# Performance work log

Measured on AMD Instinct MI355X. Metric: run time of the kernel, lower is better.

Reference implementation:

```python
import jax, jax.numpy as jnp
import numpy as np

DIM = 64
HEADS = 8
DIM_HEAD = 64
INNER = HEADS * DIM_HEAD  # 512
MLP = 256
DEPTH = 4
B = 64
HW = 15
NPATCH = HW * HW  # 225
N = NPATCH + 1    # 226 tokens incl cls
SCALE = DIM_HEAD ** -0.5
EPS = 1e-5


def setup_inputs() -> dict:
    key = jax.random.key(0)
    ks = jax.random.split(key, 20)
    s = 0.02
    inp = {
        "hsi": jax.random.normal(ks[0], (B, DIM, HW, HW), jnp.float32),
        "lidar": jax.random.normal(ks[1], (B, DIM, HW, HW), jnp.float32),
        "cls_hsi": jax.random.normal(ks[2], (1, 1, DIM), jnp.float32),
        "cls_lidar": jax.random.normal(ks[3], (1, 1, DIM), jnp.float32),
        "pos_hsi": jax.random.normal(ks[4], (1, N, DIM), jnp.float32),
        "pos_lidar": jax.random.normal(ks[5], (1, N, DIM), jnp.float32),
        "fmg_w": jax.random.normal(ks[6], (2 * DIM, DIM * DIM), jnp.float32) * s,
        "ln1_g": jnp.ones((DEPTH, DIM), jnp.float32),
        "ln1_b": jnp.zeros((DEPTH, DIM), jnp.float32),
        "qkv_w": jax.random.normal(ks[7], (DEPTH, DIM, 3 * INNER), jnp.float32) * s,
        "out_w": jax.random.normal(ks[8], (DEPTH, INNER, DIM), jnp.float32) * s,
        "out_b": jnp.zeros((DEPTH, DIM), jnp.float32),
        "ln2_g": jnp.ones((DEPTH, DIM), jnp.float32),
        "ln2_b": jnp.zeros((DEPTH, DIM), jnp.float32),
        "ff_w1": jax.random.normal(ks[9], (DEPTH, DIM, MLP), jnp.float32) * s,
        "ff_b1": jnp.zeros((DEPTH, MLP), jnp.float32),
        "ff_w2": jax.random.normal(ks[10], (DEPTH, MLP, DIM), jnp.float32) * s,
        "ff_b2": jnp.zeros((DEPTH, DIM), jnp.float32),
    }
    return inp


def _ln(x, g, b):
    m = x.mean(-1, keepdims=True)
    v = ((x - m) ** 2).mean(-1, keepdims=True)
    return (x - m) * jax.lax.rsqrt(v + EPS) * g + b


def _attn(x, dfm, g, b, wqkv, wo, bo):
    # x: [B, N, DIM]; dfm: [B, DIM_HEAD] diagonal of per-sample fusion matrix
    xn = _ln(x, g, b)
    qkv = xn @ wqkv  # [B, N, 3*INNER]
    q, k, v = jnp.split(qkv, 3, axis=-1)
    def heads(t):
        return t.reshape(B, N, HEADS, DIM_HEAD).transpose(0, 2, 1, 3)  # bhnd
    q, v = heads(q), heads(v)
    # torch.einsum('bhnd,bdd->bhnd', q, fm): repeated 'd' in bdd = diagonal of fm
    k = q * dfm[:, None, None, :]
    dots = jnp.einsum('bhid,bhjd->bhij', q, k) * SCALE
    attn = jax.nn.softmax(dots, axis=-1)
    out = jnp.einsum('bhij,bhjd->bhid', attn, v)
    out = out.transpose(0, 2, 1, 3).reshape(B, N, INNER)
    return out @ wo + bo


def _ff(x, g, b, w1, b1, w2, b2):
    xn = _ln(x, g, b)
    h = jax.nn.gelu(xn @ w1 + b1, approximate=False)
    return h @ w2 + b2


def reference(hsi, lidar, cls_hsi, cls_lidar, pos_hsi, pos_lidar, fmg_w,
              ln1_g, ln1_b, qkv_w, out_w, out_b, ln2_g, ln2_b,
              ff_w1, ff_b1, ff_w2, ff_b2):
    # patch_to_embedding with p1=p2=1: b c h w -> b (h w) c
    h_e = hsi.reshape(B, DIM, NPATCH).transpose(0, 2, 1)
    l_e = lidar.reshape(B, DIM, NPATCH).transpose(0, 2, 1)

    # fusion matrix from pre-exchange embeddings
    x = jnp.concatenate([h_e.mean(1), l_e.mean(1)], axis=-1)  # [B, 2*DIM]
    fm = jax.nn.sigmoid(x @ fmg_w).reshape(B, DIM, DIM)
    dfm = jnp.diagonal(fm, axis1=1, axis2=2)  # [B, DIM]

    # _exchange_embedding (faithful to source: reads both halves from hsi)
    n2 = NPATCH // 2
    h_ex = jnp.concatenate([h_e[:, :n2], h_e[:, n2:]], axis=1)
    l_ex = jnp.concatenate([h_e[:, :n2], h_e[:, n2:]], axis=1)

    h_ex = jnp.concatenate([jnp.broadcast_to(cls_hsi, (B, 1, DIM)), h_ex], axis=1)
    l_ex = jnp.concatenate([jnp.broadcast_to(cls_lidar, (B, 1, DIM)), l_ex], axis=1)
    h_ex = h_ex + pos_hsi[:, :N]
    l_ex = l_ex + pos_lidar[:, :N]

    def run_layers(h, l):
        for i in range(DEPTH):
            h = _attn(h, dfm, ln1_g[i], ln1_b[i], qkv_w[i], out_w[i], out_b[i]) + h
            h = _ff(h, ln2_g[i], ln2_b[i], ff_w1[i], ff_b1[i], ff_w2[i], ff_b2[i]) + h
            l = _attn(l, dfm, ln1_g[i], ln1_b[i], qkv_w[i], out_w[i], out_b[i]) + l
            l = _ff(l, ln2_g[i], ln2_b[i], ff_w1[i], ff_b1[i], ff_w2[i], ff_b2[i]) + l
        return h, l

    h_ex, l_ex = run_layers(h_ex, l_ex)

    # _exchange_token: swap cls tokens
    h_new = jnp.concatenate([l_ex[:, :1], h_ex[:, 1:]], axis=1)
    l_new = jnp.concatenate([h_ex[:, :1], l_ex[:, 1:]], axis=1)

    h_new, l_new = run_layers(h_new, l_new)
    return h_new[:, 0] + l_new[:, 0]
```

## Files before the change

### kernel.cpp

```cpp
#include <hip/hip_runtime.h>
#include <hip/hip_bf16.h>
#include <cstdint>

#define NB 64
#define ND 64
#define NH 8
#define DH 64
#define NIN 512
#define NMLP 256
#define NDEPTH 4
#define NPATCH 225
#define NTOK 226
#define NSB 128
#define NROWS (NSB*NTOK)

#define VP 240
#define PBP 40


typedef __attribute__((ext_vector_type(8))) short bfrag8;
typedef __attribute__((ext_vector_type(4))) float ffrag4;

__device__ __forceinline__ unsigned short f2b(float f) {
  uint32_t u; __builtin_memcpy(&u, &f, 4);
  u += 0x7fff + ((u >> 16) & 1);
  return (unsigned short)(u >> 16);
}

__global__ void k_dfm(const float* __restrict__ hsi, const float* __restrict__ lidar,
                      const float* __restrict__ fsub, float* __restrict__ sdfm) {
  __shared__ float xc[128];
  int b = blockIdx.x, t = threadIdx.x;
  const float* src = (t < 64) ? hsi : lidar;
  int d = t & 63;
  const float* p = src + ((size_t)b * 64 + d) * NPATCH;
  float s = 0.f;
  for (int i = 0; i < NPATCH; ++i) s += p[i];
  xc[t] = s * (1.0f / 225.0f);
  __syncthreads();
  if (t < 64) {
    float acc = 0.f;
    for (int c = 0; c < 128; ++c) acc += xc[c] * fsub[c * 64 + t];
    float sg = 1.0f / (1.0f + expf(-acc));
    sdfm[b * 64 + t] = sqrtf(sg);
  }
}

__global__ __launch_bounds__(256) void k_build(const float* __restrict__ hsi,
                        const float* __restrict__ cls_h, const float* __restrict__ cls_l,
                        const float* __restrict__ pos_h, const float* __restrict__ pos_l,
                        const float* __restrict__ g, const float* __restrict__ bb,
                        float* __restrict__ X, uint16_t* __restrict__ Xn) {
  __shared__ float Xt[113][65];
  int sb = blockIdx.x >> 1, h = blockIdx.x & 1;
  int s = sb >> 6, b = sb & 63;
  int t = threadIdx.x, w = t >> 6, l = t & 63;
  int p0 = h ? 112 : 0;
  int pc = h ? 113 : 112;

  for (int dd = 0; dd < 16; ++dd) {
    int d = w * 16 + dd;
    const float* row = hsi + ((size_t)b * 64 + d) * NPATCH + p0;
    #pragma unroll
    for (int ch = 0; ch < 2; ++ch) {
      int i = ch * 64 + l;
      if (i < pc) Xt[i][d] = row[i];
    }
  }
  __syncthreads();

  int d = l;
  for (int n_loc = w; n_loc <= 112; n_loc += 4) {
    int n = h * 113 + n_loc;
    float v;
    if (n == 0) v = s ? cls_l[d] : cls_h[d];
    else        v = Xt[h ? n_loc : (n_loc - 1)][d];
    v += (s ? pos_l : pos_h)[n * ND + d];
    size_t r = (size_t)sb * NTOK + n;
    X[r * ND + d] = v;
    float sm = v, sq = v * v;
    #pragma unroll
    for (int o = 32; o; o >>= 1) { sm += __shfl_xor(sm, o); sq += __shfl_xor(sq, o); }
    float m = sm * (1.f / 64.f);
    float rs = rsqrtf(sq * (1.f / 64.f) - m * m + 1e-5f);
    Xn[r * ND + d] = f2b((v - m) * rs * g[d] + bb[d]);
  }
}

__global__ __launch_bounds__(256) void k_wconv(
    const float* __restrict__ qkv_w, const float* __restrict__ out_w,
    const float* __restrict__ ff_w1, const float* __restrict__ ff_w2,
    const float* __restrict__ fmg_w,
    uint16_t* __restrict__ Wqv, uint16_t* __restrict__ Wo,
    uint16_t* __restrict__ W1, uint16_t* __restrict__ W2,
    float* __restrict__ fmg_sub) {
  int i = blockIdx.x * 256 + threadIdx.x;
  if (i < 262144) {
    int ly = i >> 16, rem = i & 65535, n = rem >> 6, k = rem & 63;
    int col = n + ((n >> 9) << 9);
    Wqv[i] = f2b(qkv_w[((size_t)ly * 64 + k) * 1536 + col]);
  } else if (i < 393216) {
    int j = i - 262144;
    int ly = j >> 15, rem = j & 32767, n = rem >> 9, k = rem & 511;
    Wo[j] = f2b(out_w[((size_t)ly * 512 + k) * 64 + n]);
  } else if (i < 458752) {
    int j = i - 393216;
    int ly = j >> 14, rem = j & 16383, n = rem >> 6, k = rem & 63;
    W1[j] = f2b(ff_w1[((size_t)ly * 64 + k) * 256 + n]);
  } else if (i < 524288) {
    int j = i - 458752;
    int ly = j >> 14, rem = j & 16383, n = rem >> 8, k = rem & 255;
    W2[j] = f2b(ff_w2[((size_t)ly * 256 + k) * 64 + n]);
  } else {
    int j = i - 524288;
    int c = j >> 6, t = j & 63;
    fmg_sub[j] = fmg_w[(size_t)c * 4096 + t * 65];
  }
}

__global__ __launch_bounds__(512) void k_fattn(const uint16_t* __restrict__ Xn,
    const uint16_t* __restrict__ Wqv,
    const float* __restrict__ sdfm, uint16_t* __restrict__ Og) {
  __shared__ __align__(16) uint16_t qs[240 * 64];
  __shared__ __align__(16) uint16_t vt[64 * VP];
  __shared__ __align__(16) uint16_t pb[8][16 * PBP];
  int bh = blockIdx.x;
  int sb = bh >> 3, h = bh & 7;
  int t = threadIdx.x, w = t >> 6, l = t & 63;
  int quad = l >> 4, c = l & 15;
  const uint16_t* Xb = Xn + (size_t)sb * NTOK * ND;

  float sf[4];
  #pragma unroll
  for (int dt = 0; dt < 4; ++dt)
    sf[dt] = sdfm[(sb & 63) * 64 + dt * 16 + c] * 0.35355339059327373f;

  for (int it = w; it < 15; it += 8) {
    int i0 = it * 16;
    int ri = i0 + c; if (ri > 225) ri = 225;
    bfrag8 a0 = *(const bfrag8*)(Xb + (size_t)ri * 64 + quad * 8);
    bfrag8 a1 = *(const bfrag8*)(Xb + (size_t)ri * 64 + 32 + quad * 8);
    #pragma unroll
    for (int dt = 0; dt < 4; ++dt) {
      int nq = h * 64 + dt * 16 + c;
      bfrag8 bq0 = *(const bfrag8*)(Wqv + (size_t)nq * 64 + quad * 8);
      bfrag8 bq1 = *(const bfrag8*)(Wqv + (size_t)nq * 64 + 32 + quad * 8);
      ffrag4 zq = {0.f, 0.f, 0.f, 0.f};
      zq = __builtin_amdgcn_mfma_f32_16x16x32_bf16(a0, bq0, zq, 0, 0, 0);
      zq = __builtin_amdgcn_mfma_f32_16x16x32_bf16(a1, bq1, zq, 0, 0, 0);
      bfrag8 bv0 = *(const bfrag8*)(Wqv + (size_t)(512 + nq) * 64 + quad * 8);
      bfrag8 bv1 = *(const bfrag8*)(Wqv + (size_t)(512 + nq) * 64 + 32 + quad * 8);
      ffrag4 zv = {0.f, 0.f, 0.f, 0.f};
      zv = __builtin_amdgcn_mfma_f32_16x16x32_bf16(a0, bv0, zv, 0, 0, 0);
      zv = __builtin_amdgcn_mfma_f32_16x16x32_bf16(a1, bv1, zv, 0, 0, 0);
      int d = dt * 16 + c;
      #pragma unroll
      for (int r = 0; r < 4; ++r) {
        int i = i0 + quad * 4 + r;
        qs[i * 64 + ((((d >> 3) ^ (i & 7))) << 3) + (d & 7)] = f2b(zq[r] * sf[dt]);
        vt[d * VP + i] = f2b(zv[r]);
      }
    }
  }
  __syncthreads();

  uint16_t* pw = &pb[w][0];
  for (int it = w; it < 15; it += 8) {
    int i0 = it * 16;
    int ra = i0 + c, sa = ra & 7;
    bfrag8 a0 = *(const bfrag8*)(qs + ra * 64 + ((quad ^ sa) << 3));
    bfrag8 a1 = *(const bfrag8*)(qs + ra * 64 + (((quad + 4) ^ sa) << 3));
    ffrag4 acc[15];
    #pragma unroll
    for (int jt = 0; jt < 15; ++jt) {
      int rb = jt * 16 + c, sk = rb & 7;
      bfrag8 b0 = *(const bfrag8*)(qs + rb * 64 + ((quad ^ sk) << 3));
      bfrag8 b1 = *(const bfrag8*)(qs + rb * 64 + (((quad + 4) ^ sk) << 3));
      ffrag4 z = {0.f, 0.f, 0.f, 0.f};
      z = __builtin_amdgcn_mfma_f32_16x16x32_bf16(a0, b0, z, 0, 0, 0);
      z = __builtin_amdgcn_mfma_f32_16x16x32_bf16(a1, b1, z, 0, 0, 0);
      acc[jt] = z;
    }
    float rinv[4];
    #pragma unroll
    for (int r = 0; r < 4; ++r) {
      float m = -1e30f;
      #pragma unroll
      for (int jt = 0; jt < 15; ++jt) m = fmaxf(m, acc[jt][r]);
      #pragma unroll
      for (int o = 8; o; o >>= 1) m = fmaxf(m, __shfl_xor(m, o));
      float s = 0.f;
      #pragma unroll
      for (int jt = 0; jt < 15; ++jt) {
        float p = __expf(acc[jt][r] - m);
        if (jt == 14 && c >= 2) p = 0.f;
        acc[jt][r] = p;
        s += p;
      }
      #pragma unroll
      for (int o = 8; o; o >>= 1) s += __shfl_xor(s, o);
      rinv[r] = 1.f / s;
    }
    ffrag4 oa[4];
    #pragma unroll
    for (int dt = 0; dt < 4; ++dt) oa[dt] = (ffrag4){0.f, 0.f, 0.f, 0.f};
    for (int jc = 0; jc < 8; ++jc) {
      if (jc == 7) {
        *(unsigned long long*)(pw + c * PBP + 16 + quad * 4) = 0ull;
      }
      #pragma unroll
      for (int r = 0; r < 4; ++r) {
        int row = quad * 4 + r;
        pw[row * PBP + c] = f2b(acc[2 * jc][r]);
        if (jc < 7) pw[row * PBP + 16 + c] = f2b(acc[2 * jc + 1][r]);
      }
      bfrag8 pa = *(const bfrag8*)(pw + c * PBP + quad * 8);
      int j0 = jc * 32;
      #pragma unroll
      for (int dt = 0; dt < 4; ++dt) {
        bfrag8 vb;
        if (jc < 7)
          vb = *(const bfrag8*)(vt + (dt * 16 + c) * VP + j0 + quad * 8);
        else
          vb = *(const bfrag8*)(vt + (dt * 16 + c) * VP + 224 + (quad & 1) * 8);
        oa[dt] = __builtin_amdgcn_mfma_f32_16x16x32_bf16(pa, vb, oa[dt], 0, 0, 0);
      }
    }
    #pragma unroll
    for (int dt = 0; dt < 4; ++dt) {
      #pragma unroll
      for (int r = 0; r < 4; ++r) {
        int i = i0 + quad * 4 + r;
        if (i < NTOK)
          Og[((size_t)sb * NTOK + i) * NIN + h * DH + dt * 16 + c] =
              f2b(oa[dt][r] * rinv[r]);
      }
    }
  }
}

__global__ __launch_bounds__(128) void k_pf(const uint16_t* __restrict__ Og,
    const uint16_t* __restrict__ Wot,
    const float* __restrict__ bo, float* __restrict__ X,
    const float* __restrict__ g2, const float* __restrict__ bb2,
    const uint16_t* __restrict__ W1t,
    const float* __restrict__ b1,
    const uint16_t* __restrict__ W2t,
    const float* __restrict__ b2,
    const float* __restrict__ gn, const float* __restrict__ bbn,
    uint16_t* __restrict__ XnOut) {
  __shared__ __align__(16) uint16_t xa2[16 * 72];
  __shared__ __align__(16) uint16_t ha[16 * 264];
  __shared__ float lnp[2][16][2];
  int t = threadIdx.x;
  int w = t >> 6, l = t & 63;
  int quad = l >> 4, c = l & 15;
  int r0 = blockIdx.x * 16;

  const uint16_t* orow = Og + (size_t)(r0 + c) * 512 + quad * 8;
  bfrag8 a[16];
  #pragma unroll
  for (int kc = 0; kc < 16; ++kc) a[kc] = *(const bfrag8*)(orow + kc * 32);
  ffrag4 acc[2][2];
  #pragma unroll
  for (int j = 0; j < 2; ++j)
    #pragma unroll
    for (int p = 0; p < 2; ++p) acc[j][p] = (ffrag4){0.f, 0.f, 0.f, 0.f};
  #pragma unroll
  for (int kc = 0; kc < 16; ++kc) {
    #pragma unroll
    for (int j = 0; j < 2; ++j) {
      int jt = 2 * w + j;
      bfrag8 b = *(const bfrag8*)(Wot + (size_t)(jt * 16 + c) * 512 + kc * 32 + quad * 8);
      acc[j][kc & 1] = __builtin_amdgcn_mfma_f32_16x16x32_bf16(a[kc], b, acc[j][kc & 1], 0, 0, 0);
    }
  }
  float xv[2][4];
  #pragma unroll
  for (int j = 0; j < 2; ++j) {
    int jt = 2 * w + j;
    float bv = bo[jt * 16 + c];
    #pragma unroll
    for (int r = 0; r < 4; ++r) {
      int il = quad * 4 + r;
      size_t idx = (size_t)(r0 + il) * 64 + jt * 16 + c;
      xv[j][r] = X[idx] + (acc[j][0][r] + acc[j][1][r]) + bv;
    }
  }
  #pragma unroll
  for (int r = 0; r < 4; ++r) {
    float s = xv[0][r] + xv[1][r];
    float q = xv[0][r] * xv[0][r] + xv[1][r] * xv[1][r];
    #pragma unroll
    for (int o = 8; o; o >>= 1) { s += __shfl_xor(s, o); q += __shfl_xor(q, o); }
    if (c == 0) { lnp[w][quad * 4 + r][0] = s; lnp[w][quad * 4 + r][1] = q; }
  }
  __syncthreads();
  #pragma unroll
  for (int r = 0; r < 4; ++r) {
    int il = quad * 4 + r;
    float s = lnp[0][il][0] + lnp[1][il][0];
    float q = lnp[0][il][1] + lnp[1][il][1];
    float m = s * (1.f / 64.f);
    float rs = rsqrtf(q * (1.f / 64.f) - m * m + 1e-5f);
    #pragma unroll
    for (int j = 0; j < 2; ++j) {
      int n = (2 * w + j) * 16 + c;
      xa2[il * 72 + n] = f2b((xv[j][r] - m) * rs * g2[n] + bb2[n]);
    }
  }
  __syncthreads();
  const uint16_t* xrow = xa2 + c * 72;
  bfrag8 a0 = *(const bfrag8*)(xrow + quad * 8);
  bfrag8 a1 = *(const bfrag8*)(xrow + 32 + quad * 8);
  #pragma unroll
  for (int jj = 0; jj < 8; ++jj) {
    int jt = 8 * w + jj;
    bfrag8 b0  = *(const bfrag8*)(W1t + (size_t)(jt * 16 + c) * 64 + quad * 8);
    bfrag8 b1f = *(const bfrag8*)(W1t + (size_t)(jt * 16 + c) * 64 + 32 + quad * 8);
    ffrag4 z = {0.f, 0.f, 0.f, 0.f};
    z = __builtin_amdgcn_mfma_f32_16x16x32_bf16(a0, b0, z, 0, 0, 0);
    z = __builtin_amdgcn_mfma_f32_16x16x32_bf16(a1, b1f, z, 0, 0, 0);
    float bv = b1[jt * 16 + c];
    #pragma unroll
    for (int r = 0; r < 4; ++r) {
      float zz = z[r] + bv;
      float hg = 0.5f * zz * (1.f + erff(zz * 0.7071067811865476f));
      ha[(quad * 4 + r) * 264 + jt * 16 + c] = f2b(hg);
    }
  }
  __syncthreads();
  ffrag4 o2[2][2];
  #pragma unroll
  for (int j = 0; j < 2; ++j)
    #pragma unroll
    for (int p = 0; p < 2; ++p) o2[j][p] = (ffrag4){0.f, 0.f, 0.f, 0.f};
  #pragma unroll
  for (int kc = 0; kc < 8; ++kc) {
    bfrag8 pa = *(const bfrag8*)(ha + c * 264 + kc * 32 + quad * 8);
    #pragma unroll
    for (int j = 0; j < 2; ++j) {
      int jt = 2 * w + j;
      bfrag8 vb = *(const bfrag8*)(W2t + (size_t)(jt * 16 + c) * 256 + kc * 32 + quad * 8);
      o2[j][kc & 1] = __builtin_amdgcn_mfma_f32_16x16x32_bf16(pa, vb, o2[j][kc & 1], 0, 0, 0);
    }
  }
  float yv[2][4];
  #pragma unroll
  for (int j = 0; j < 2; ++j) {
    int jt = 2 * w + j;
    float bv = b2[jt * 16 + c];
    #pragma unroll
    for (int r = 0; r < 4; ++r) {
      int il = quad * 4 + r;
      size_t idx = (size_t)(r0 + il) * 64 + jt * 16 + c;
      float v = xv[j][r] + (o2[j][0][r] + o2[j][1][r]) + bv;
      X[idx] = v;
      yv[j][r] = v;
    }
  }
  #pragma unroll
  for (int r = 0; r < 4; ++r) {
    float s = yv[0][r] + yv[1][r];
    float q = yv[0][r] * yv[0][r] + yv[1][r] * yv[1][r];
    #pragma unroll
    for (int o = 8; o; o >>= 1) { s += __shfl_xor(s, o); q += __shfl_xor(q, o); }
    if (c == 0) { lnp[w][quad * 4 + r][0] = s; lnp[w][quad * 4 + r][1] = q; }
  }
  __syncthreads();
  #pragma unroll
  for (int r = 0; r < 4; ++r) {
    int il = quad * 4 + r;
    float s = lnp[0][il][0] + lnp[1][il][0];
    float q = lnp[0][il][1] + lnp[1][il][1];
    float m = s * (1.f / 64.f);
    float rs = rsqrtf(q * (1.f / 64.f) - m * m + 1e-5f);
    #pragma unroll
    for (int j = 0; j < 2; ++j) {
      int n = (2 * w + j) * 16 + c;
      XnOut[(size_t)(r0 + il) * 64 + n] = f2b((yv[j][r] - m) * rs * gn[n] + bbn[n]);
    }
  }
}

__global__ void k_xchg(float* __restrict__ X, uint16_t* __restrict__ Xn,
                       const float* __restrict__ g, const float* __restrict__ bb) {
  int b = blockIdx.x, d = threadIdx.x;
  size_t i0 = (size_t)(b * NTOK) * ND + d;
  size_t i1 = (size_t)((64 + b) * NTOK) * ND + d;
  float a = X[i0], cc = X[i1];
  X[i0] = cc; X[i1] = a;
  float s0 = cc, q0 = cc * cc, s1 = a, q1 = a * a;
  #pragma unroll
  for (int o = 32; o; o >>= 1) {
    s0 += __shfl_xor(s0, o); q0 += __shfl_xor(q0, o);
    s1 += __shfl_xor(s1, o); q1 += __shfl_xor(q1, o);
  }
  float m0 = s0 * (1.f / 64.f), rs0 = rsqrtf(q0 * (1.f / 64.f) - m0 * m0 + 1e-5f);
  float m1 = s1 * (1.f / 64.f), rs1 = rsqrtf(q1 * (1.f / 64.f) - m1 * m1 + 1e-5f);
  Xn[i0] = f2b((cc - m0) * rs0 * g[d] + bb[d]);
  Xn[i1] = f2b((a - m1) * rs1 * g[d] + bb[d]);
}

__global__ void k_out(const float* __restrict__ X, float* __restrict__ out) {
  int i = blockIdx.x * 64 + threadIdx.x;
  int b = i >> 6, d = i & 63;
  out[i] = X[(size_t)b * NTOK * ND + d] + X[(size_t)(64 + b) * NTOK * ND + d];
}

extern "C" void kernel_launch(void* const* d_in, const int* in_sizes, int n_in,
                              void* d_out, int out_size, void* d_ws, size_t ws_size,
                              hipStream_t stream) {
  const float* hsi   = (const float*)d_in[0];
  const float* lidar = (const float*)d_in[1];
  const float* cls_h = (const float*)d_in[2];
  const float* cls_l = (const float*)d_in[3];
  const float* pos_h = (const float*)d_in[4];
  const float* pos_l = (const float*)d_in[5];
  const float* fmg_w = (const float*)d_in[6];
  const float* ln1_g = (const float*)d_in[7];
  const float* ln1_b = (const float*)d_in[8];
  const float* qkv_w = (const float*)d_in[9];
  const float* out_w = (const float*)d_in[10];
  const float* out_b = (const float*)d_in[11];
  const float* ln2_g = (const float*)d_in[12];
  const float* ln2_b = (const float*)d_in[13];
  const float* ff_w1 = (const float*)d_in[14];
  const float* ff_b1 = (const float*)d_in[15];
  const float* ff_w2 = (const float*)d_in[16];
  const float* ff_b2 = (const float*)d_in[17];

  char* ws = (char*)d_ws;
  float*    X    = (float*)ws;
  float*    sdfm = (float*)(ws + 7405568);
  uint16_t* Xn   = (uint16_t*)(ws + 7421952);
  uint16_t* Og   = (uint16_t*)(ws + 11124736);
  uint16_t* Wqv  = (uint16_t*)(ws + 40747008);
  uint16_t* Wo   = (uint16_t*)(ws + 41271296);
  uint16_t* W1   = (uint16_t*)(ws + 41533440);
  uint16_t* W2   = (uint16_t*)(ws + 41664512);
  float* fmg_sub = (float*)(ws + 11124736);

  k_wconv<<<2080, 256, 0, stream>>>(qkv_w, out_w, ff_w1, ff_w2, fmg_w,
                                    Wqv, Wo, W1, W2, fmg_sub);
  k_dfm<<<NB, 128, 0, stream>>>(hsi, lidar, fmg_sub, sdfm);
  k_build<<<NSB * 2, 256, 0, stream>>>(hsi, cls_h, cls_l, pos_h, pos_l,
                                       ln1_g, ln1_b, X, Xn);
  for (int pass = 0; pass < 2; ++pass) {
    for (int ly = 0; ly < NDEPTH; ++ly) {
      int nx = (ly + 1) & 3;
      k_fattn<<<NSB * NH, 512, 0, stream>>>(Xn, Wqv + (size_t)ly * 65536, sdfm, Og);
      k_pf<<<NROWS / 16, 128, 0, stream>>>(Og, Wo + (size_t)ly * 32768, out_b + ly * ND,
                                           X, ln2_g + ly * ND, ln2_b + ly * ND,
                                           W1 + (size_t)ly * 16384, ff_b1 + ly * NMLP,
                                           W2 + (size_t)ly * 16384, ff_b2 + ly * ND,
                                           ln1_g + nx * ND, ln1_b + nx * ND, Xn);
    }
    if (pass == 0) k_xchg<<<64, 64, 0, stream>>>(X, Xn, ln1_g, ln1_b);
  }
  k_out<<<64, 64, 0, stream>>>(X, (float*)d_out);
}
```

Measured before the change: 808.3 us.

## Merge setup kernels into one launch and use two-chunk online softmax in attention

The weight conversion, fusion-diagonal and token-build kernels are merged into a single launch whose blocks branch by index, and the dfm block now reads fmg_w directly instead of a staged copy. This removes two launches and an intermediate buffer. Separately, the attention kernel now computes scores in two chunks of 8 and 7 tiles with an online-softmax rescale, which cuts the accumulator registers needed per wave. That may raise occupancy, at the cost of extra exp and rescale work.

```diff
diff --git a/kernel.cpp b/kernel.cpp
--- a/kernel.cpp
+++ b/kernel.cpp
@@ -27,94 +27,90 @@
   return (unsigned short)(u >> 16);
 }
 
-__global__ void k_dfm(const float* __restrict__ hsi, const float* __restrict__ lidar,
-                      const float* __restrict__ fsub, float* __restrict__ sdfm) {
-  __shared__ float xc[128];
-  int b = blockIdx.x, t = threadIdx.x;
-  const float* src = (t < 64) ? hsi : lidar;
-  int d = t & 63;
-  const float* p = src + ((size_t)b * 64 + d) * NPATCH;
-  float s = 0.f;
-  for (int i = 0; i < NPATCH; ++i) s += p[i];
-  xc[t] = s * (1.0f / 225.0f);
-  __syncthreads();
-  if (t < 64) {
-    float acc = 0.f;
-    for (int c = 0; c < 128; ++c) acc += xc[c] * fsub[c * 64 + t];
-    float sg = 1.0f / (1.0f + expf(-acc));
-    sdfm[b * 64 + t] = sqrtf(sg);
-  }
-}
-
-__global__ __launch_bounds__(256) void k_build(const float* __restrict__ hsi,
-                        const float* __restrict__ cls_h, const float* __restrict__ cls_l,
-                        const float* __restrict__ pos_h, const float* __restrict__ pos_l,
-                        const float* __restrict__ g, const float* __restrict__ bb,
-                        float* __restrict__ X, uint16_t* __restrict__ Xn) {
-  __shared__ float Xt[113][65];
-  int sb = blockIdx.x >> 1, h = blockIdx.x & 1;
-  int s = sb >> 6, b = sb & 63;
-  int t = threadIdx.x, w = t >> 6, l = t & 63;
-  int p0 = h ? 112 : 0;
-  int pc = h ? 113 : 112;
-
-  for (int dd = 0; dd < 16; ++dd) {
-    int d = w * 16 + dd;
-    const float* row = hsi + ((size_t)b * 64 + d) * NPATCH + p0;
-    #pragma unroll
-    for (int ch = 0; ch < 2; ++ch) {
-      int i = ch * 64 + l;
-      if (i < pc) Xt[i][d] = row[i];
-    }
-  }
-  __syncthreads();
-
-  int d = l;
-  for (int n_loc = w; n_loc <= 112; n_loc += 4) {
-    int n = h * 113 + n_loc;
-    float v;
-    if (n == 0) v = s ? cls_l[d] : cls_h[d];
-    else        v = Xt[h ? n_loc : (n_loc - 1)][d];
-    v += (s ? pos_l : pos_h)[n * ND + d];
-    size_t r = (size_t)sb * NTOK + n;
-    X[r * ND + d] = v;
-    float sm = v, sq = v * v;
-    #pragma unroll
-    for (int o = 32; o; o >>= 1) { sm += __shfl_xor(sm, o); sq += __shfl_xor(sq, o); }
-    float m = sm * (1.f / 64.f);
-    float rs = rsqrtf(sq * (1.f / 64.f) - m * m + 1e-5f);
-    Xn[r * ND + d] = f2b((v - m) * rs * g[d] + bb[d]);
-  }
-}
-
-__global__ __launch_bounds__(256) void k_wconv(
+__global__ __launch_bounds__(256) void k_setup(
     const float* __restrict__ qkv_w, const float* __restrict__ out_w,
     const float* __restrict__ ff_w1, const float* __restrict__ ff_w2,
     const float* __restrict__ fmg_w,
+    const float* __restrict__ hsi, const float* __restrict__ lidar,
+    const float* __restrict__ cls_h, const float* __restrict__ cls_l,
+    const float* __restrict__ pos_h, const float* __restrict__ pos_l,
+    const float* __restrict__ g, const float* __restrict__ bb,
     uint16_t* __restrict__ Wqv, uint16_t* __restrict__ Wo,
     uint16_t* __restrict__ W1, uint16_t* __restrict__ W2,
-    float* __restrict__ fmg_sub) {
-  int i = blockIdx.x * 256 + threadIdx.x;
-  if (i < 262144) {
-    int ly = i >> 16, rem = i & 65535, n = rem >> 6, k = rem & 63;
-    int col = n + ((n >> 9) << 9);
-    Wqv[i] = f2b(qkv_w[((size_t)ly * 64 + k) * 1536 + col]);
-  } else if (i < 393216) {
-    int j = i - 262144;
-    int ly = j >> 15, rem = j & 32767, n = rem >> 9, k = rem & 511;
-    Wo[j] = f2b(out_w[((size_t)ly * 512 + k) * 64 + n]);
-  } else if (i < 458752) {
-    int j = i - 393216;
-    int ly = j >> 14, rem = j & 16383, n = rem >> 6, k = rem & 63;
-    W1[j] = f2b(ff_w1[((size_t)ly * 64 + k) * 256 + n]);
-  } else if (i < 524288) {
-    int j = i - 458752;
-    int ly = j >> 14, rem = j & 16383, n = rem >> 8, k = rem & 255;
-    W2[j] = f2b(ff_w2[((size_t)ly * 256 + k) * 64 + n]);
+    float* __restrict__ sdfm, float* __restrict__ X, uint16_t* __restrict__ Xn) {
+  __shared__ float Xt[113][65];
+  __shared__ float xc[2][128];
+  int blk = blockIdx.x, t = threadIdx.x;
+
+  if (blk < 2048) {
+    int i = blk * 256 + t;
+    if (i < 262144) {
+      int ly = i >> 16, rem = i & 65535, n = rem >> 6, k = rem & 63;
+      int col = n + ((n >> 9) << 9);
+      Wqv[i] = f2b(qkv_w[((size_t)ly * 64 + k) * 1536 + col]);
+    } else if (i < 393216) {
+      int j = i - 262144;
+      int ly = j >> 15, rem = j & 32767, n = rem >> 9, k = rem & 511;
+      Wo[j] = f2b(out_w[((size_t)ly * 512 + k) * 64 + n]);
+    } else if (i < 458752) {
+      int j = i - 393216;
+      int ly = j >> 14, rem = j & 16383, n = rem >> 6, k = rem & 63;
+      W1[j] = f2b(ff_w1[((size_t)ly * 64 + k) * 256 + n]);
+    } else {
+      int j = i - 458752;
+      int ly = j >> 14, rem = j & 16383, n = rem >> 8, k = rem & 255;
+      W2[j] = f2b(ff_w2[((size_t)ly * 256 + k) * 64 + n]);
+    }
+  } else if (blk < 2080) {
+    int gsel = t >> 7, tt = t & 127;
+    int b = (blk - 2048) * 2 + gsel;
+    const float* src = (tt < 64) ? hsi : lidar;
+    int d = tt & 63;
+    const float* p = src + ((size_t)b * 64 + d) * NPATCH;
+    float s = 0.f;
+    for (int i = 0; i < NPATCH; ++i) s += p[i];
+    xc[gsel][tt] = s * (1.0f / 225.0f);
+    __syncthreads();
+    if (tt < 64) {
+      float acc = 0.f;
+      const float* w = fmg_w + tt * 65;
+      for (int c = 0; c < 128; ++c) acc += xc[gsel][c] * w[c * 4096];
+      float sg = 1.0f / (1.0f + expf(-acc));
+      sdfm[b * 64 + tt] = sqrtf(sg);
+    }
   } else {
-    int j = i - 524288;
-    int c = j >> 6, t = j & 63;
-    fmg_sub[j] = fmg_w[(size_t)c * 4096 + t * 65];
+    int bidx = blk - 2080;
+    int sb = bidx >> 1, h = bidx & 1;
+    int s = sb >> 6, b = sb & 63;
+    int w = t >> 6, l = t & 63;
+    int p0 = h ? 112 : 0;
+    int pc = h ? 113 : 112;
+    for (int dd = 0; dd < 16; ++dd) {
+      int d = w * 16 + dd;
+      const float* row = hsi + ((size_t)b * 64 + d) * NPATCH + p0;
+      #pragma unroll
+      for (int ch = 0; ch < 2; ++ch) {
+        int i = ch * 64 + l;
+        if (i < pc) Xt[i][d] = row[i];
+      }
+    }
+    __syncthreads();
+    int d = l;
+    for (int n_loc = w; n_loc <= 112; n_loc += 4) {
+      int n = h * 113 + n_loc;
+      float v;
+      if (n == 0) v = s ? cls_l[d] : cls_h[d];
+      else        v = Xt[h ? n_loc : (n_loc - 1)][d];
+      v += (s ? pos_l : pos_h)[n * ND + d];
+      size_t r = (size_t)sb * NTOK + n;
+      X[r * ND + d] = v;
+      float sm = v, sq = v * v;
+      #pragma unroll
+      for (int o = 32; o; o >>= 1) { sm += __shfl_xor(sm, o); sq += __shfl_xor(sq, o); }
+      float m = sm * (1.f / 64.f);
+      float rs = rsqrtf(sq * (1.f / 64.f) - m * m + 1e-5f);
+      Xn[r * ND + d] = f2b((v - m) * rs * g[d] + bb[d]);
+    }
   }
 }
 
@@ -170,60 +166,79 @@
     int ra = i0 + c, sa = ra & 7;
     bfrag8 a0 = *(const bfrag8*)(qs + ra * 64 + ((quad ^ sa) << 3));
     bfrag8 a1 = *(const bfrag8*)(qs + ra * 64 + (((quad + 4) ^ sa) << 3));
-    ffrag4 acc[15];
-    #pragma unroll
-    for (int jt = 0; jt < 15; ++jt) {
-      int rb = jt * 16 + c, sk = rb & 7;
-      bfrag8 b0 = *(const bfrag8*)(qs + rb * 64 + ((quad ^ sk) << 3));
-      bfrag8 b1 = *(const bfrag8*)(qs + rb * 64 + (((quad + 4) ^ sk) << 3));
-      ffrag4 z = {0.f, 0.f, 0.f, 0.f};
-      z = __builtin_amdgcn_mfma_f32_16x16x32_bf16(a0, b0, z, 0, 0, 0);
-      z = __builtin_amdgcn_mfma_f32_16x16x32_bf16(a1, b1, z, 0, 0, 0);
-      acc[jt] = z;
-    }
-    float rinv[4];
-    #pragma unroll
-    for (int r = 0; r < 4; ++r) {
-      float m = -1e30f;
-      #pragma unroll
-      for (int jt = 0; jt < 15; ++jt) m = fmaxf(m, acc[jt][r]);
-      #pragma unroll
-      for (int o = 8; o; o >>= 1) m = fmaxf(m, __shfl_xor(m, o));
-      float s = 0.f;
-      #pragma unroll
-      for (int jt = 0; jt < 15; ++jt) {
-        float p = __expf(acc[jt][r] - m);
-        if (jt == 14 && c >= 2) p = 0.f;
-        acc[jt][r] = p;
-        s += p;
-      }
-      #pragma unroll
-      for (int o = 8; o; o >>= 1) s += __shfl_xor(s, o);
-      rinv[r] = 1.f / s;
-    }
+    float mrun[4], srun[4];
     ffrag4 oa[4];
     #pragma unroll
     for (int dt = 0; dt < 4; ++dt) oa[dt] = (ffrag4){0.f, 0.f, 0.f, 0.f};
-    for (int jc = 0; jc < 8; ++jc) {
-      if (jc == 7) {
-        *(unsigned long long*)(pw + c * PBP + 16 + quad * 4) = 0ull;
-      }
+
+    #pragma unroll
+    for (int ch = 0; ch < 2; ++ch) {
+      const int nt = ch ? 7 : 8;
+      ffrag4 acc[8];
+      #pragma unroll
+      for (int k = 0; k < nt; ++k) {
+        int jt = ch * 8 + k;
+        int rb = jt * 16 + c, sk = rb & 7;
+        bfrag8 b0 = *(const bfrag8*)(qs + rb * 64 + ((quad ^ sk) << 3));
+        bfrag8 b1 = *(const bfrag8*)(qs + rb * 64 + (((quad + 4) ^ sk) << 3));
+        ffrag4 z = {0.f, 0.f, 0.f, 0.f};
+        z = __builtin_amdgcn_mfma_f32_16x16x32_bf16(a0, b0, z, 0, 0, 0);
+        z = __builtin_amdgcn_mfma_f32_16x16x32_bf16(a1, b1, z, 0, 0, 0);
+        acc[k] = z;
+      }
+      float scale[4];
       #pragma unroll
       for (int r = 0; r < 4; ++r) {
-        int row = quad * 4 + r;
-        pw[row * PBP + c] = f2b(acc[2 * jc][r]);
-        if (jc < 7) pw[row * PBP + 16 + c] = f2b(acc[2 * jc + 1][r]);
-      }
-      bfrag8 pa = *(const bfrag8*)(pw + c * PBP + quad * 8);
-      int j0 = jc * 32;
-      #pragma unroll
-      for (int dt = 0; dt < 4; ++dt) {
-        bfrag8 vb;
-        if (jc < 7)
-          vb = *(const bfrag8*)(vt + (dt * 16 + c) * VP + j0 + quad * 8);
-        else
-          vb = *(const bfrag8*)(vt + (dt * 16 + c) * VP + 224 + (quad & 1) * 8);
-        oa[dt] = __builtin_amdgcn_mfma_f32_16x16x32_bf16(pa, vb, oa[dt], 0, 0, 0);
+        float mloc = -1e30f;
+        #pragma unroll
+        for (int k = 0; k < nt; ++k) mloc = fmaxf(mloc, acc[k][r]);
+        #pragma unroll
+        for (int o = 8; o; o >>= 1) mloc = fmaxf(mloc, __shfl_xor(mloc, o));
+        float mnew = ch ? fmaxf(mrun[r], mloc) : mloc;
+        scale[r] = ch ? __expf(mrun[r] - mnew) : 1.f;
+        float s = 0.f;
+        #pragma unroll
+        for (int k = 0; k < nt; ++k) {
+          int jt = ch * 8 + k;
+          float p = __expf(acc[k][r] - mnew);
+          if (jt == 14 && c >= 2) p = 0.f;
+          acc[k][r] = p;
+          s += p;
+        }
+        #pragma unroll
+        for (int o = 8; o; o >>= 1) s += __shfl_xor(s, o);
+        srun[r] = ch ? srun[r] * scale[r] + s : s;
+        mrun[r] = mnew;
+      }
+      if (ch) {
+        #pragma unroll
+        for (int dt = 0; dt < 4; ++dt)
+          #pragma unroll
+          for (int r = 0; r < 4; ++r) oa[dt][r] *= scale[r];
+      }
+      #pragma unroll
+      for (int jl = 0; jl < 4; ++jl) {
+        int jc = ch * 4 + jl;
+        if (jc == 7) {
+          *(unsigned long long*)(pw + c * PBP + 16 + quad * 4) = 0ull;
+        }
+        #pragma unroll
+        for (int r = 0; r < 4; ++r) {
+          int row = quad * 4 + r;
+          pw[row * PBP + c] = f2b(acc[2 * jl][r]);
+          if (jc < 7) pw[row * PBP + 16 + c] = f2b(acc[2 * jl + 1][r]);
+        }
+        bfrag8 pa = *(const bfrag8*)(pw + c * PBP + quad * 8);
+        int j0 = jc * 32;
+        #pragma unroll
+        for (int dt = 0; dt < 4; ++dt) {
+          bfrag8 vb;
+          if (jc < 7)
+            vb = *(const bfrag8*)(vt + (dt * 16 + c) * VP + j0 + quad * 8);
+          else
+            vb = *(const bfrag8*)(vt + (dt * 16 + c) * VP + 224 + (quad & 1) * 8);
+          oa[dt] = __builtin_amdgcn_mfma_f32_16x16x32_bf16(pa, vb, oa[dt], 0, 0, 0);
+        }
       }
     }
     #pragma unroll
@@ -233,7 +248,7 @@
         int i = i0 + quad * 4 + r;
         if (i < NTOK)
           Og[((size_t)sb * NTOK + i) * NIN + h * DH + dt * 16 + c] =
-              f2b(oa[dt][r] * rinv[r]);
+              f2b(oa[dt][r] * (1.f / srun[r]));
       }
     }
   }
@@ -439,13 +454,11 @@
   uint16_t* Wo   = (uint16_t*)(ws + 41271296);
   uint16_t* W1   = (uint16_t*)(ws + 41533440);
   uint16_t* W2   = (uint16_t*)(ws + 41664512);
-  float* fmg_sub = (float*)(ws + 11124736);
-
-  k_wconv<<<2080, 256, 0, stream>>>(qkv_w, out_w, ff_w1, ff_w2, fmg_w,
-                                    Wqv, Wo, W1, W2, fmg_sub);
-  k_dfm<<<NB, 128, 0, stream>>>(hsi, lidar, fmg_sub, sdfm);
-  k_build<<<NSB * 2, 256, 0, stream>>>(hsi, cls_h, cls_l, pos_h, pos_l,
-                                       ln1_g, ln1_b, X, Xn);
+
+  k_setup<<<2336, 256, 0, stream>>>(qkv_w, out_w, ff_w1, ff_w2, fmg_w,
+                                    hsi, lidar, cls_h, cls_l, pos_h, pos_l,
+                                    ln1_g, ln1_b,
+                                    Wqv, Wo, W1, W2, sdfm, X, Xn);
   for (int pass = 0; pass < 2; ++pass) {
     for (int ly = 0; ly < NDEPTH; ++ly) {
       int nx = (ly + 1) & 3;
```

After: 839.7 us. 1.04x slower.
